# Optimization experiments

Hardware: AMD Instinct MI355X
Metric: run time of the kernel (lower is better)

## Reference

```python
import jax, jax.numpy as jnp
import numpy as np


def _l2norm(t, axis=-1, eps=1e-12):
    # matches torch F.normalize: x / max(||x||, eps)
    n = jnp.sqrt(jnp.sum(t * t, axis=axis, keepdims=True))
    return t / jnp.maximum(n, eps)


def setup_inputs() -> dict:
    key = jax.random.key(0)
    ks = jax.random.split(key, 5)
    B, N, C, H = 16, 4096, 768, 12
    x = jax.random.normal(ks[0], (B, N, C), dtype=jnp.float32)
    Wqkv = jax.random.normal(ks[1], (C, 3 * C), dtype=jnp.float32) * (C ** -0.5)
    bqkv = jax.random.normal(ks[2], (3 * C,), dtype=jnp.float32) * 0.02
    Wproj = jax.random.normal(ks[3], (C, C), dtype=jnp.float32) * (C ** -0.5)
    bproj = jax.random.normal(ks[4], (C,), dtype=jnp.float32) * 0.02
    temperature = jnp.ones((H, 1, 1), dtype=jnp.float32)
    return {"x": x, "Wqkv": Wqkv, "bqkv": bqkv, "Wproj": Wproj,
            "bproj": bproj, "temperature": temperature}


def reference(x, Wqkv, bqkv, Wproj, bproj, temperature):
    B, N, C = x.shape
    H = temperature.shape[0]
    Dh = C // H
    qkv = x @ Wqkv + bqkv                      # [B,N,3C]
    qkv = qkv.reshape(B, N, 3, H, Dh)
    # -> [3,B,H,Dh,N] (channels-as-tokens layout)
    qkv = jnp.transpose(qkv, (2, 0, 3, 4, 1))
    q, k, v = qkv[0], qkv[1], qkv[2]           # each [B,H,Dh,N]
    q = _l2norm(q, axis=-1)
    k = _l2norm(k, axis=-1)
    # cross-covariance over channels: [B,H,Dh,Dh]
    attn = jnp.einsum('bhdn,bhen->bhde', q, k) * temperature
    attn = jax.nn.softmax(attn, axis=-1)
    out = jnp.einsum('bhde,bhen->bhdn', attn, v)  # [B,H,Dh,N]
    out = jnp.transpose(out, (0, 3, 1, 2)).reshape(B, N, C)
    return out @ Wproj + bproj
```

## Files before the change

kernel.cpp:

```cpp
#include <hip/hip_runtime.h>

typedef __bf16 bf16x8 __attribute__((ext_vector_type(8)));
typedef float  f32x4  __attribute__((ext_vector_type(4)));
typedef unsigned short u16x8 __attribute__((ext_vector_type(8)));
typedef unsigned short u16x4 __attribute__((ext_vector_type(4)));

#define MFMA16(a, b, c) __builtin_amdgcn_mfma_f32_16x16x32_bf16((a), (b), (c), 0, 0, 0)

#define GLOAD16(g, l) __builtin_amdgcn_global_load_lds( \
    (const __attribute__((address_space(1))) void*)(g),  \
    (__attribute__((address_space(3))) void*)(l), 16, 0, 0)

__device__ __forceinline__ float bf2f(unsigned short u) {
    unsigned int x = ((unsigned int)u) << 16;
    return __builtin_bit_cast(float, x);
}
__device__ __forceinline__ unsigned short f2bf(float f) {
    unsigned int x = __builtin_bit_cast(unsigned int, f);
    x = x + 0x7FFFu + ((x >> 16) & 1u);
    return (unsigned short)(x >> 16);
}
__device__ __forceinline__ bool is_f32(const unsigned short* tf) { return tf[0] == 0; }
__device__ __forceinline__ float ldscal(const void* p, int i, bool f32m) {
    return f32m ? ((const float*)p)[i] : bf2f(((const unsigned short*)p)[i]);
}

__global__ __launch_bounds__(256)
void conv_x(const void* __restrict__ in, unsigned short* __restrict__ out,
            const unsigned short* __restrict__ tf)
{
    const bool f32m = is_f32(tf);
    const int n8 = 6291456;
    for (int i = blockIdx.x * 256 + threadIdx.x; i < n8; i += gridDim.x * 256) {
        u16x8 v;
        if (f32m) {
            const float* p = (const float*)in + (size_t)i * 8;
            f32x4 a = *(const f32x4*)p;
            f32x4 b = *(const f32x4*)(p + 4);
#pragma unroll
            for (int j = 0; j < 4; ++j) { v[j] = f2bf(a[j]); v[4 + j] = f2bf(b[j]); }
        } else {
            v = *(const u16x8*)((const unsigned short*)in + (size_t)i * 8);
        }
        *(u16x8*)&out[(size_t)i * 8] = v;
    }
}

__global__ __launch_bounds__(256)
void tr_conv(const void* __restrict__ in_, unsigned short* __restrict__ out,
             int R, int C, int istride, const unsigned short* __restrict__ tf)
{
    __shared__ unsigned short T[64 * 72];
    const bool f32m = is_f32(tf);
    const int nct = C >> 6;
    const int tx = blockIdx.x % nct;
    const int ty = blockIdx.x / nct;
    const int r0 = ty * 64, c0 = tx * 64;
    const int t = threadIdx.x;
#pragma unroll
    for (int s = 0; s < 2; ++s) {
        const int idx = t + s * 256;
        const int rr = idx >> 3;
        const int cc = (idx & 7) * 8;
        unsigned short v[8];
        if (f32m) {
            const float* inf = (const float*)in_;
            f32x4 a = *(const f32x4*)&inf[(size_t)(r0 + rr) * istride + c0 + cc];
            f32x4 b = *(const f32x4*)&inf[(size_t)(r0 + rr) * istride + c0 + cc + 4];
#pragma unroll
            for (int j = 0; j < 4; ++j) { v[j] = f2bf(a[j]); v[4 + j] = f2bf(b[j]); }
        } else {
            u16x8 a = *(const u16x8*)&((const unsigned short*)in_)[(size_t)(r0 + rr) * istride + c0 + cc];
#pragma unroll
            for (int j = 0; j < 8; ++j) v[j] = a[j];
        }
#pragma unroll
        for (int j = 0; j < 8; ++j) T[(cc + j) * 72 + rr] = v[j];
    }
    __syncthreads();
#pragma unroll
    for (int s = 0; s < 2; ++s) {
        const int idx = t + s * 256;
        const int cc = idx >> 3;
        const int rr = (idx & 7) * 8;
        u16x8 v = *(const u16x8*)&T[cc * 72 + rr];
        *(u16x8*)&out[(size_t)(c0 + cc) * R + r0 + rr] = v;
    }
}

__global__ __launch_bounds__(256)
void conv_wv(const void* __restrict__ Wqkv, unsigned short* __restrict__ Wv_bf,
             const unsigned short* __restrict__ tf)
{
    const bool f32m = is_f32(tf);
    const int t = blockIdx.x * 256 + threadIdx.x;
    const int c = t / 96;
    const int e0 = (t % 96) * 8;
    u16x8 v;
    if (f32m) {
        const float* p = (const float*)Wqkv + (size_t)c * 2304 + 1536 + e0;
        f32x4 a = *(const f32x4*)p;
        f32x4 b = *(const f32x4*)(p + 4);
#pragma unroll
        for (int j = 0; j < 4; ++j) { v[j] = f2bf(a[j]); v[4 + j] = f2bf(b[j]); }
    } else {
        v = *(const u16x8*)&((const unsigned short*)Wqkv)[(size_t)c * 2304 + 1536 + e0];
    }
    *(u16x8*)&Wv_bf[(size_t)c * 768 + e0] = v;
}

template<int MODE>
__global__ __launch_bounds__(512, 2)
void gemm256(const unsigned short* __restrict__ A,
             const unsigned short* __restrict__ BT,
             const void* __restrict__ bias,
             unsigned short* __restrict__ o0,
             unsigned short* __restrict__ o1,
             float* __restrict__ oF,
             const unsigned short* __restrict__ tf)
{
    constexpr int K = 768, NT = 12;
    constexpr int NB = (MODE == 0) ? 6 : 3;
    constexpr int LDSSZ = (MODE == 0) ? 135168 : 131072;
    __shared__ __align__(16) char SM[LDSSZ];

    const bool f32m = is_f32(tf);
    const int tid  = threadIdx.x;
    const int wave = tid >> 6;
    const int lane = tid & 63;
    const int wm   = wave >> 2;
    const int wn   = wave & 3;
    const int lr   = lane & 15;
    const int lq   = lane >> 4;
    const int sw16 = ((lq ^ (lr & 3)) << 4);

    const int per = gridDim.x >> 3;
    const int wg  = (blockIdx.x & 7) * per + (blockIdx.x >> 3);
    const int mt  = wg / NB;
    const int nt  = wg % NB;
    const size_t m0 = (size_t)mt * 256;
    const int n0 = nt * 256;

    const unsigned short* Bt = BT + ((MODE == 1) ? ((m0 >> 12) * (size_t)589824) : (size_t)0);

    f32x4 zero = {0.f, 0.f, 0.f, 0.f};
    f32x4 acc[8][4];
#pragma unroll
    for (int i = 0; i < 8; ++i)
#pragma unroll
        for (int j = 0; j < 4; ++j) acc[i][j] = zero;

    auto STAGE_EV = [&](int mat, int kh, int t) {
        const unsigned short* g = mat ? (Bt + (size_t)n0 * K) : (A + m0 * K);
        char* dst = SM + (t & 1) * 65536 + mat * 32768 + kh * 16384;
#pragma unroll
        for (int ev = 0; ev < 2; ++ev) {
            const int c = ev * 512 + tid;
            const int row = c >> 2;
            const int sg  = (c & 3) ^ (row & 3);
            GLOAD16(g + (size_t)row * K + t * 64 + kh * 32 + sg * 8, dst + c * 16);
        }
    };

    STAGE_EV(0, 0, 0); STAGE_EV(1, 0, 0);
    STAGE_EV(0, 1, 0); STAGE_EV(1, 1, 0);
    STAGE_EV(0, 0, 1); STAGE_EV(1, 0, 1);

    bf16x8 af[4], bfr[4];

#define READ_B(ks) do { \
    _Pragma("unroll") for (int ni = 0; ni < 4; ++ni) \
        bfr[ni] = *(const bf16x8*)(lb + (ks) * 16384 + (wn * 64 + ni * 16 + lr) * 64 + sw16); } while (0)
#define READ_A(mh, ks) do { \
    _Pragma("unroll") for (int mi = 0; mi < 4; ++mi) \
        af[mi] = *(const bf16x8*)(la + (ks) * 16384 + (wm * 128 + (mh) * 64 + mi * 16 + lr) * 64 + sw16); } while (0)
#define MFMA_Q(mh) do { \
    _Pragma("unroll") for (int mi = 0; mi < 4; ++mi) \
    _Pragma("unroll") for (int ni = 0; ni < 4; ++ni) \
        acc[(mh) * 4 + mi][ni] = MFMA16(af[mi], bfr[ni], acc[(mh) * 4 + mi][ni]); } while (0)
#define PH_MID() do { \
    __builtin_amdgcn_sched_barrier(0); \
    __builtin_amdgcn_s_barrier(); \
    asm volatile("s_waitcnt lgkmcnt(0)" ::: "memory"); \
    __builtin_amdgcn_sched_barrier(0); } while (0)
#define PH_END() do { \
    __builtin_amdgcn_sched_barrier(0); \
    __builtin_amdgcn_s_barrier(); } while (0)

    for (int t = 0; t < NT; ++t) {
        const char* la = (const char*)SM + (t & 1) * 65536;
        const char* lb = la + 32768;

        if (t < NT - 1) asm volatile("s_waitcnt vmcnt(8)" ::: "memory");
        else            asm volatile("s_waitcnt vmcnt(4)" ::: "memory");
        __builtin_amdgcn_s_barrier();
        __builtin_amdgcn_sched_barrier(0);

        READ_B(0); READ_A(0, 0);
        if (t + 1 < NT) STAGE_EV(0, 1, t + 1);
        PH_MID();
        __builtin_amdgcn_s_setprio(1); MFMA_Q(0); __builtin_amdgcn_s_setprio(0);
        PH_END();

        READ_A(1, 0);
        if (t + 1 < NT) STAGE_EV(1, 1, t + 1);
        if (t < NT - 1) asm volatile("s_waitcnt vmcnt(8)" ::: "memory");
        else            asm volatile("s_waitcnt vmcnt(0)" ::: "memory");
        PH_MID();
        __builtin_amdgcn_s_setprio(1); MFMA_Q(1); __builtin_amdgcn_s_setprio(0);
        PH_END();

        READ_B(1); READ_A(0, 1);
        if (t + 2 < NT) STAGE_EV(0, 0, t + 2);
        PH_MID();
        __builtin_amdgcn_s_setprio(1); MFMA_Q(0); __builtin_amdgcn_s_setprio(0);
        PH_END();

        READ_A(1, 1);
        if (t + 2 < NT) STAGE_EV(1, 0, t + 2);
        PH_MID();
        __builtin_amdgcn_s_setprio(1); MFMA_Q(1); __builtin_amdgcn_s_setprio(0);
        PH_END();
    }
#undef READ_B
#undef READ_A
#undef MFMA_Q
#undef PH_MID
#undef PH_END

    asm volatile("s_waitcnt lgkmcnt(0)" ::: "memory");
    __builtin_amdgcn_s_barrier();

    float bb[4];
#pragma unroll
    for (int ni = 0; ni < 4; ++ni) {
        const int col = n0 + wn * 64 + ni * 16 + lr;
        if (MODE == 0)      bb[ni] = ldscal(bias, col, f32m);
        else if (MODE == 1) bb[ni] = ((const float*)bias)[(m0 >> 12) * 768 + col];
        else                bb[ni] = 0.f;
    }

    if (MODE == 1 || MODE == 2) {
#pragma unroll
        for (int mi = 0; mi < 8; ++mi)
#pragma unroll
            for (int ni = 0; ni < 4; ++ni)
#pragma unroll
                for (int r = 0; r < 4; ++r) {
                    const size_t row = m0 + (size_t)(wm * 128 + mi * 16 + lq * 4 + r);
                    const int col = n0 + wn * 64 + ni * 16 + lr;
                    const float val = acc[mi][ni][r] + bb[ni];
                    if (MODE == 2)      o0[row * 768 + col] = f2bf(val);
                    else if (f32m)      oF[row * 768 + col] = val;
                    else                o0[row * 768 + col] = f2bf(val);
                }
    } else {
        unsigned short* CTw = (unsigned short*)SM + wave * (64 * 132);
        const int cbase = (n0 < 768) ? n0 : (n0 - 768);
        unsigned short* dst = (n0 < 768) ? o0 : o1;
        const int h = (cbase >> 6) + wn;
        const size_t bh = (m0 >> 12) * 12 + h;
        const int tokbase = (int)(m0 & 4095) + wm * 128;
#pragma unroll
        for (int mi = 0; mi < 8; ++mi)
#pragma unroll
            for (int ni = 0; ni < 4; ++ni) {
                u16x4 pk;
#pragma unroll
                for (int r = 0; r < 4; ++r) pk[r] = f2bf(acc[mi][ni][r] + bb[ni]);
                *(u16x4*)&CTw[(ni * 16 + lr) * 132 + mi * 16 + lq * 4] = pk;
            }
#pragma unroll
        for (int rep = 0; rep < 16; ++rep) {
            const int d = rep * 4 + lq;
            u16x8 v = *(const u16x8*)&CTw[d * 132 + lr * 8];
            *(u16x8*)&dst[(bh * 64 + d) * 4096 + tokbase + lr * 8] = v;
        }
    }
}

__global__ __launch_bounds__(256)
void attn_sm(const unsigned short* __restrict__ qt,
             const unsigned short* __restrict__ ktb,
             const unsigned short* __restrict__ tf,
             unsigned short* __restrict__ attnT)
{
    __shared__ float S[64][64];
    __shared__ float nq[64];
    __shared__ float nk[64];
    const bool f32m = is_f32(tf);
    const int bh = blockIdx.x;
    const int h = bh % 12;
    const unsigned short* Q  = qt  + (size_t)bh * (64 * 4096);
    const unsigned short* Kp = ktb + (size_t)bh * (64 * 4096);
    const int tid = threadIdx.x;
    const int wave = tid >> 6;
    const int lane = tid & 63;
    if (tid < 64) { nq[tid] = 0.f; nk[tid] = 0.f; }

    f32x4 zero = {0.f, 0.f, 0.f, 0.f};
    f32x4 acc[4][4];
#pragma unroll
    for (int i = 0; i < 4; ++i)
#pragma unroll
        for (int j = 0; j < 4; ++j) acc[i][j] = zero;
    f32x4 gq[4], gk[4];
#pragma unroll
    for (int i = 0; i < 4; ++i) { gq[i] = zero; gk[i] = zero; }

    const int lr = lane & 15;
    const int lq = lane >> 4;
    const int lk = lq * 8;

    for (int it = 0; it < 32; ++it) {
        const int nb = (it * 4 + wave) * 32 + lk;
        u16x8 qa[4], ka[4];
#pragma unroll
        for (int mi = 0; mi < 4; ++mi)
            qa[mi] = *(const u16x8*)&Q[(size_t)(mi * 16 + lr) * 4096 + nb];
#pragma unroll
        for (int ni = 0; ni < 4; ++ni)
            ka[ni] = *(const u16x8*)&Kp[(size_t)(ni * 16 + lr) * 4096 + nb];
#pragma unroll
        for (int mi = 0; mi < 4; ++mi) {
            gq[mi] = MFMA16(__builtin_bit_cast(bf16x8, qa[mi]),
                            __builtin_bit_cast(bf16x8, qa[mi]), gq[mi]);
            gk[mi] = MFMA16(__builtin_bit_cast(bf16x8, ka[mi]),
                            __builtin_bit_cast(bf16x8, ka[mi]), gk[mi]);
        }
#pragma unroll
        for (int mi = 0; mi < 4; ++mi)
#pragma unroll
            for (int ni = 0; ni < 4; ++ni)
                acc[mi][ni] = MFMA16(__builtin_bit_cast(bf16x8, qa[mi]),
                                     __builtin_bit_cast(bf16x8, ka[ni]),
                                     acc[mi][ni]);
    }

    for (int ww = 0; ww < 4; ++ww) {
        if (wave == ww) {
#pragma unroll
            for (int mi = 0; mi < 4; ++mi)
#pragma unroll
                for (int ni = 0; ni < 4; ++ni)
#pragma unroll
                    for (int r = 0; r < 4; ++r) {
                        const int d = mi * 16 + lq * 4 + r;
                        const int e = ni * 16 + lr;
                        if (ww == 0) S[d][e] = acc[mi][ni][r];
                        else         S[d][e] += acc[mi][ni][r];
                    }
        }
        __syncthreads();
    }

    {
        const int rdiag = lr - lq * 4;
        if (rdiag >= 0 && rdiag < 4) {
#pragma unroll
            for (int mi = 0; mi < 4; ++mi) {
                atomicAdd(&nq[mi * 16 + lr], gq[mi][rdiag]);
                atomicAdd(&nk[mi * 16 + lr], gk[mi][rdiag]);
            }
        }
    }
    __syncthreads();

    const int d  = tid >> 2;
    const int qq = tid & 3;
    const float tv = f32m ? ((const float*)tf)[h] : bf2f(tf[h]);
    const float qn = fmaxf(sqrtf(nq[d]), 1e-12f);
    float vals[16];
    float mx = -1e30f;
#pragma unroll
    for (int i = 0; i < 16; ++i) {
        const int e = qq * 16 + i;
        const float s = S[d][e] / (qn * fmaxf(sqrtf(nk[e]), 1e-12f)) * tv;
        vals[i] = s;
        mx = fmaxf(mx, s);
    }
    mx = fmaxf(mx, __shfl_xor(mx, 1));
    mx = fmaxf(mx, __shfl_xor(mx, 2));
    float sum = 0.f;
#pragma unroll
    for (int i = 0; i < 16; ++i) { vals[i] = __expf(vals[i] - mx); sum += vals[i]; }
    sum += __shfl_xor(sum, 1);
    sum += __shfl_xor(sum, 2);
    const float inv = 1.0f / sum;
#pragma unroll
    for (int i = 0; i < 16; ++i) {
        const int e = qq * 16 + i;
        attnT[(size_t)bh * 4096 + e * 64 + d] = f2bf(vals[i] * inv);
    }
}

__global__ __launch_bounds__(512)
void mb_build(const unsigned short* __restrict__ attnT,
              const unsigned short* __restrict__ WprojT,
              unsigned short* __restrict__ MbT)
{
    const int bh = blockIdx.x;
    const int b = bh / 12, h = bh % 12;
    const int tid = threadIdx.x;
    const int wave = tid >> 6;
    const int lane = tid & 63;
    const unsigned short* At = attnT + (size_t)bh * 4096;

    f32x4 zero = {0.f, 0.f, 0.f, 0.f};
    f32x4 acc[4][6];
#pragma unroll
    for (int i = 0; i < 4; ++i)
#pragma unroll
        for (int j = 0; j < 6; ++j) acc[i][j] = zero;

    const int lr  = lane & 15;
    const int lk8 = (lane >> 4) * 8;

#pragma unroll
    for (int ks = 0; ks < 2; ++ks) {
        bf16x8 af[4], bfr[6];
#pragma unroll
        for (int mi = 0; mi < 4; ++mi)
            af[mi] = *(const bf16x8*)&At[(mi * 16 + lr) * 64 + ks * 32 + lk8];
#pragma unroll
        for (int ni = 0; ni < 6; ++ni) {
            const int j = wave * 96 + ni * 16 + lr;
            bfr[ni] = *(const bf16x8*)&WprojT[(size_t)j * 768 + h * 64 + ks * 32 + lk8];
        }
#pragma unroll
        for (int mi = 0; mi < 4; ++mi)
#pragma unroll
            for (int ni = 0; ni < 6; ++ni)
                acc[mi][ni] = MFMA16(af[mi], bfr[ni], acc[mi][ni]);
    }

#pragma unroll
    for (int mi = 0; mi < 4; ++mi)
#pragma unroll
        for (int ni = 0; ni < 6; ++ni) {
            const int e = mi * 16 + (lane >> 4) * 4;
            const int j = wave * 96 + ni * 16 + lr;
            u16x4 pk;
#pragma unroll
            for (int r = 0; r < 4; ++r) pk[r] = f2bf(acc[mi][ni][r]);
            *(u16x4*)&MbT[(size_t)b * 589824 + (size_t)j * 768 + h * 64 + e] = pk;
        }
}

__global__ __launch_bounds__(256)
void beff_k(const unsigned short* __restrict__ MbT,
            const void* __restrict__ bqkv, const void* __restrict__ bp,
            float* __restrict__ beff, const unsigned short* __restrict__ tf)
{
    __shared__ float bv[768];
    const bool f32m = is_f32(tf);
    for (int i = threadIdx.x; i < 768; i += 256) bv[i] = ldscal(bqkv, 1536 + i, f32m);
    __syncthreads();
    const int t = blockIdx.x * 256 + threadIdx.x;
    const int b = t / 768, j = t % 768;
    float s = ldscal(bp, j, f32m);
    const unsigned short* row = MbT + (size_t)b * 589824 + (size_t)j * 768;
    for (int e8 = 0; e8 < 96; ++e8) {
        u16x8 m = *(const u16x8*)&row[e8 * 8];
#pragma unroll
        for (int jj = 0; jj < 8; ++jj) s += bf2f(m[jj]) * bv[e8 * 8 + jj];
    }
    beff[t] = s;
}

extern "C" void kernel_launch(void* const* d_in, const int* in_sizes, int n_in,
                              void* d_out, int out_size, void* d_ws, size_t ws_size,
                              hipStream_t stream)
{
    const void* x    = d_in[0];
    const void* Wqkv = d_in[1];
    const void* bqkv = d_in[2];
    const void* Wp   = d_in[3];
    const void* bp   = d_in[4];
    const unsigned short* tf = (const unsigned short*)d_in[5];

    char* w = (char*)d_ws;
    unsigned short* qt     = (unsigned short*)(w);
    unsigned short* PT     = (unsigned short*)(w);
    float*          beff   = (float*)(w + 18874368);
    unsigned short* ktb    = (unsigned short*)(w + 100663296);
    unsigned short* xb     = (unsigned short*)(w + 201326592);
    unsigned short* WqkT   = (unsigned short*)(w + 301989888);
    unsigned short* Wv_bf  = (unsigned short*)(w + 304349184);
    unsigned short* attnT  = (unsigned short*)(w + 305528832);
    unsigned short* MbT    = (unsigned short*)(w + 307101696);
    unsigned short* WprojT = (unsigned short*)(w + 325976064);

    conv_x <<<dim3(2048), dim3(256), 0, stream>>>(x, xb, tf);
    tr_conv<<<dim3(288),  dim3(256), 0, stream>>>(Wqkv, WqkT, 768, 1536, 2304, tf);
    conv_wv<<<dim3(288),  dim3(256), 0, stream>>>(Wqkv, Wv_bf, tf);
    tr_conv<<<dim3(144),  dim3(256), 0, stream>>>(Wp, WprojT, 768, 768, 768, tf);

    gemm256<0><<<dim3(1536), dim3(512), 0, stream>>>(xb, WqkT, bqkv, qt, ktb, nullptr, tf);
    attn_sm<<<dim3(192), dim3(256), 0, stream>>>(qt, ktb, tf, attnT);
    mb_build<<<dim3(192), dim3(512), 0, stream>>>(attnT, WprojT, MbT);
    gemm256<2><<<dim3(144), dim3(512), 0, stream>>>(MbT, Wv_bf, nullptr, PT, nullptr, nullptr, tf);
    beff_k<<<dim3(48), dim3(256), 0, stream>>>(MbT, bqkv, bp, beff, tf);
    gemm256<1><<<dim3(768), dim3(512), 0, stream>>>(xb, PT, beff,
        (unsigned short*)d_out, nullptr, (float*)d_out, tf);
}
```

Before: 473.2 us.

## Compute q·k cross-covariance via per-batch Gram matrix instead of materialising Q and K

```diff
diff --git a/kernel.cpp b/kernel.cpp
--- a/kernel.cpp
+++ b/kernel.cpp
@@ -26,23 +26,42 @@
 }
 
 __global__ __launch_bounds__(256)
-void conv_x(const void* __restrict__ in, unsigned short* __restrict__ out,
-            const unsigned short* __restrict__ tf)
-{
+void tr_dual(const void* __restrict__ in_, unsigned short* __restrict__ xb,
+             unsigned short* __restrict__ xbT, const unsigned short* __restrict__ tf)
+{
+    __shared__ unsigned short T[64 * 72];
     const bool f32m = is_f32(tf);
-    const int n8 = 6291456;
-    for (int i = blockIdx.x * 256 + threadIdx.x; i < n8; i += gridDim.x * 256) {
+    const int tx = blockIdx.x % 12;
+    const int ty = blockIdx.x / 12;
+    const int r0 = ty * 64, c0 = tx * 64;
+    const int t = threadIdx.x;
+#pragma unroll
+    for (int s = 0; s < 2; ++s) {
+        const int idx = t + s * 256;
+        const int rr = idx >> 3;
+        const int cc = (idx & 7) * 8;
         u16x8 v;
         if (f32m) {
-            const float* p = (const float*)in + (size_t)i * 8;
-            f32x4 a = *(const f32x4*)p;
-            f32x4 b = *(const f32x4*)(p + 4);
+            const float* inf = (const float*)in_;
+            f32x4 a = *(const f32x4*)&inf[(size_t)(r0 + rr) * 768 + c0 + cc];
+            f32x4 b = *(const f32x4*)&inf[(size_t)(r0 + rr) * 768 + c0 + cc + 4];
 #pragma unroll
             for (int j = 0; j < 4; ++j) { v[j] = f2bf(a[j]); v[4 + j] = f2bf(b[j]); }
         } else {
-            v = *(const u16x8*)((const unsigned short*)in + (size_t)i * 8);
-        }
-        *(u16x8*)&out[(size_t)i * 8] = v;
+            v = *(const u16x8*)&((const unsigned short*)in_)[(size_t)(r0 + rr) * 768 + c0 + cc];
+        }
+        *(u16x8*)&xb[(size_t)(r0 + rr) * 768 + c0 + cc] = v;
+#pragma unroll
+        for (int j = 0; j < 8; ++j) T[(cc + j) * 72 + rr] = v[j];
+    }
+    __syncthreads();
+#pragma unroll
+    for (int s = 0; s < 2; ++s) {
+        const int idx = t + s * 256;
+        const int cc = idx >> 3;
+        const int rr = (idx & 7) * 8;
+        u16x8 v = *(const u16x8*)&T[cc * 72 + rr];
+        *(u16x8*)&xbT[(size_t)(c0 + cc) * 65536 + r0 + rr] = v;
     }
 }
 
@@ -109,20 +128,40 @@
     *(u16x8*)&Wv_bf[(size_t)c * 768 + e0] = v;
 }
 
+__global__ __launch_bounds__(256)
+void colsum(const unsigned short* __restrict__ xbT, float* __restrict__ s)
+{
+    const int b = blockIdx.x / 12;
+    const int jg = blockIdx.x % 12;
+    const int tid = threadIdx.x;
+    const int d = tid >> 2;
+    const int seg = tid & 3;
+    const int j = jg * 64 + d;
+    const unsigned short* p = xbT + (size_t)j * 65536 + b * 4096 + seg * 1024;
+    float acc = 0.f;
+    for (int i = 0; i < 128; ++i) {
+        u16x8 v = *(const u16x8*)&p[i * 8];
+#pragma unroll
+        for (int k = 0; k < 8; ++k) acc += bf2f(v[k]);
+    }
+    acc += __shfl_xor(acc, 1);
+    acc += __shfl_xor(acc, 2);
+    if (seg == 0) s[b * 768 + j] = acc;
+}
+
 template<int MODE>
 __global__ __launch_bounds__(512, 2)
 void gemm256(const unsigned short* __restrict__ A,
              const unsigned short* __restrict__ BT,
-             const void* __restrict__ bias,
+             const float* __restrict__ bias,
              unsigned short* __restrict__ o0,
-             unsigned short* __restrict__ o1,
              float* __restrict__ oF,
              const unsigned short* __restrict__ tf)
 {
-    constexpr int K = 768, NT = 12;
-    constexpr int NB = (MODE == 0) ? 6 : 3;
-    constexpr int LDSSZ = (MODE == 0) ? 135168 : 131072;
-    __shared__ __align__(16) char SM[LDSSZ];
+    constexpr int NT = (MODE == 3) ? 64 : 12;
+    constexpr size_t LDA = (MODE == 3) ? 65536 : 768;
+    constexpr size_t LDB = (MODE == 3) ? 65536 : 768;
+    __shared__ __align__(16) char SM[131072];
 
     const bool f32m = is_f32(tf);
     const int tid  = threadIdx.x;
@@ -132,16 +171,28 @@
     const int wn   = wave & 3;
     const int lr   = lane & 15;
     const int lq   = lane >> 4;
-    const int sw16 = ((lq ^ (lr & 3)) << 4);
+    const int lrh  = lr >> 1;
+    const int pA   = (((lr & 1) << 2) | lq) ^ lrh;
 
     const int per = gridDim.x >> 3;
     const int wg  = (blockIdx.x & 7) * per + (blockIdx.x >> 3);
-    const int mt  = wg / NB;
-    const int nt  = wg % NB;
+    int b = 0, mt, nt;
+    if (MODE == 3)      { b = wg / 9;  const int r = wg % 9;  mt = r / 3; nt = r % 3; }
+    else if (MODE == 4) { b = wg / 18; const int r = wg % 18; mt = r / 3; nt = r % 3; }
+    else                { mt = wg / 3; nt = wg % 3; }
     const size_t m0 = (size_t)mt * 256;
     const int n0 = nt * 256;
 
-    const unsigned short* Bt = BT + ((MODE == 1) ? ((m0 >> 12) * (size_t)589824) : (size_t)0);
+    const unsigned short* Ab;
+    const unsigned short* Bb;
+    if (MODE == 3)      { Ab = A + m0 * LDA + (size_t)b * 4096;
+                          Bb = A + (size_t)n0 * LDA + (size_t)b * 4096; }
+    else if (MODE == 4) { Ab = A + m0 * LDA;
+                          Bb = BT + (size_t)b * 589824 + (size_t)n0 * LDB; }
+    else if (MODE == 1) { Ab = A + m0 * LDA;
+                          Bb = BT + (m0 >> 12) * (size_t)589824 + (size_t)n0 * LDB; }
+    else                { Ab = A + m0 * LDA;
+                          Bb = BT + (size_t)n0 * LDB; }
 
     f32x4 zero = {0.f, 0.f, 0.f, 0.f};
     f32x4 acc[8][4];
@@ -151,14 +202,17 @@
         for (int j = 0; j < 4; ++j) acc[i][j] = zero;
 
     auto STAGE_EV = [&](int mat, int kh, int t) {
-        const unsigned short* g = mat ? (Bt + (size_t)n0 * K) : (A + m0 * K);
+        const unsigned short* g = mat ? Bb : Ab;
+        const size_t ld = mat ? LDB : LDA;
         char* dst = SM + (t & 1) * 65536 + mat * 32768 + kh * 16384;
 #pragma unroll
         for (int ev = 0; ev < 2; ++ev) {
             const int c = ev * 512 + tid;
-            const int row = c >> 2;
-            const int sg  = (c & 3) ^ (row & 3);
-            GLOAD16(g + (size_t)row * K + t * 64 + kh * 32 + sg * 8, dst + c * 16);
+            const int rp = c >> 3;
+            const int chunk = (c & 7) ^ (rp & 7);
+            const int srow = rp * 2 + (chunk >> 2);
+            const int sk = kh * 32 + (chunk & 3) * 8;
+            GLOAD16(g + (size_t)srow * ld + t * 64 + sk, dst + c * 16);
         }
     };
 
@@ -170,10 +224,10 @@
 
 #define READ_B(ks) do { \
     _Pragma("unroll") for (int ni = 0; ni < 4; ++ni) \
-        bfr[ni] = *(const bf16x8*)(lb + (ks) * 16384 + (wn * 64 + ni * 16 + lr) * 64 + sw16); } while (0)
+        bfr[ni] = *(const bf16x8*)(lb + (ks) * 16384 + (wn * 32 + ni * 8 + lrh) * 128 + pA * 16); } while (0)
 #define READ_A(mh, ks) do { \
     _Pragma("unroll") for (int mi = 0; mi < 4; ++mi) \
-        af[mi] = *(const bf16x8*)(la + (ks) * 16384 + (wm * 128 + (mh) * 64 + mi * 16 + lr) * 64 + sw16); } while (0)
+        af[mi] = *(const bf16x8*)(la + (ks) * 16384 + (wm * 64 + (mh) * 32 + mi * 8 + lrh) * 128 + pA * 16); } while (0)
 #define MFMA_Q(mh) do { \
     _Pragma("unroll") for (int mi = 0; mi < 4; ++mi) \
     _Pragma("unroll") for (int ni = 0; ni < 4; ++ni) \
@@ -228,75 +282,62 @@
 #undef PH_MID
 #undef PH_END
 
-    asm volatile("s_waitcnt lgkmcnt(0)" ::: "memory");
-    __builtin_amdgcn_s_barrier();
-
     float bb[4];
 #pragma unroll
     for (int ni = 0; ni < 4; ++ni) {
         const int col = n0 + wn * 64 + ni * 16 + lr;
-        if (MODE == 0)      bb[ni] = ldscal(bias, col, f32m);
-        else if (MODE == 1) bb[ni] = ((const float*)bias)[(m0 >> 12) * 768 + col];
-        else                bb[ni] = 0.f;
-    }
-
-    if (MODE == 1 || MODE == 2) {
-#pragma unroll
-        for (int mi = 0; mi < 8; ++mi)
-#pragma unroll
-            for (int ni = 0; ni < 4; ++ni)
-#pragma unroll
-                for (int r = 0; r < 4; ++r) {
-                    const size_t row = m0 + (size_t)(wm * 128 + mi * 16 + lq * 4 + r);
-                    const int col = n0 + wn * 64 + ni * 16 + lr;
-                    const float val = acc[mi][ni][r] + bb[ni];
-                    if (MODE == 2)      o0[row * 768 + col] = f2bf(val);
-                    else if (f32m)      oF[row * 768 + col] = val;
-                    else                o0[row * 768 + col] = f2bf(val);
+        bb[ni] = (MODE == 1) ? bias[(m0 >> 12) * 768 + col] : 0.f;
+    }
+
+#pragma unroll
+    for (int mi = 0; mi < 8; ++mi)
+#pragma unroll
+        for (int ni = 0; ni < 4; ++ni)
+#pragma unroll
+            for (int r = 0; r < 4; ++r) {
+                const size_t row = m0 + (size_t)(wm * 128 + mi * 16 + lq * 4 + r);
+                const int col = n0 + wn * 64 + ni * 16 + lr;
+                const float val = acc[mi][ni][r] + bb[ni];
+                if (MODE == 1) {
+                    if (f32m) oF[row * 768 + col] = val;
+                    else      o0[row * 768 + col] = f2bf(val);
+                } else if (MODE == 2) {
+                    o0[row * 768 + col] = f2bf(val);
+                } else if (MODE == 3) {
+                    o0[(size_t)b * 589824 + row * 768 + col] = f2bf(val);
+                } else {
+                    o0[(size_t)b * 1179648 + row * 768 + col] = f2bf(val);
                 }
-    } else {
-        unsigned short* CTw = (unsigned short*)SM + wave * (64 * 132);
-        const int cbase = (n0 < 768) ? n0 : (n0 - 768);
-        unsigned short* dst = (n0 < 768) ? o0 : o1;
-        const int h = (cbase >> 6) + wn;
-        const size_t bh = (m0 >> 12) * 12 + h;
-        const int tokbase = (int)(m0 & 4095) + wm * 128;
-#pragma unroll
-        for (int mi = 0; mi < 8; ++mi)
-#pragma unroll
-            for (int ni = 0; ni < 4; ++ni) {
-                u16x4 pk;
-#pragma unroll
-                for (int r = 0; r < 4; ++r) pk[r] = f2bf(acc[mi][ni][r] + bb[ni]);
-                *(u16x4*)&CTw[(ni * 16 + lr) * 132 + mi * 16 + lq * 4] = pk;
             }
-#pragma unroll
-        for (int rep = 0; rep < 16; ++rep) {
-            const int d = rep * 4 + lq;
-            u16x8 v = *(const u16x8*)&CTw[d * 132 + lr * 8];
-            *(u16x8*)&dst[(bh * 64 + d) * 4096 + tokbase + lr * 8] = v;
-        }
-    }
 }
 
 __global__ __launch_bounds__(256)
-void attn_sm(const unsigned short* __restrict__ qt,
-             const unsigned short* __restrict__ ktb,
-             const unsigned short* __restrict__ tf,
-             unsigned short* __restrict__ attnT)
+void attn2(const unsigned short* __restrict__ P,
+           const unsigned short* __restrict__ WqkT,
+           const float* __restrict__ s,
+           const void* __restrict__ bqkv,
+           const unsigned short* __restrict__ tf,
+           unsigned short* __restrict__ attnT)
 {
     __shared__ float S[64][64];
-    __shared__ float nq[64];
-    __shared__ float nk[64];
+    __shared__ float nq[64], nk[64], uq[64], uk[64];
+    __shared__ float sb[768];
+    __shared__ float bkv[64];
     const bool f32m = is_f32(tf);
     const int bh = blockIdx.x;
-    const int h = bh % 12;
-    const unsigned short* Q  = qt  + (size_t)bh * (64 * 4096);
-    const unsigned short* Kp = ktb + (size_t)bh * (64 * 4096);
+    const int b = bh / 12, h = bh % 12;
+    const unsigned short* Pq = P + (size_t)b * 1179648 + (size_t)(h * 64) * 768;
+    const unsigned short* Pk = Pq + 768 * 768;
+    const unsigned short* Wq = WqkT + (size_t)(h * 64) * 768;
+    const unsigned short* Wk = Wq + 768 * 768;
     const int tid = threadIdx.x;
     const int wave = tid >> 6;
     const int lane = tid & 63;
-    if (tid < 64) { nq[tid] = 0.f; nk[tid] = 0.f; }
+    const int lr = lane & 15;
+    const int lq = lane >> 4;
+
+    for (int i = tid; i < 768; i += 256) sb[i] = s[b * 768 + i];
+    if (tid < 64) bkv[tid] = ldscal(bqkv, 768 + h * 64 + tid, f32m);
 
     f32x4 zero = {0.f, 0.f, 0.f, 0.f};
     f32x4 acc[4][4];
@@ -304,30 +345,16 @@
     for (int i = 0; i < 4; ++i)
 #pragma unroll
         for (int j = 0; j < 4; ++j) acc[i][j] = zero;
-    f32x4 gq[4], gk[4];
-#pragma unroll
-    for (int i = 0; i < 4; ++i) { gq[i] = zero; gk[i] = zero; }
-
-    const int lr = lane & 15;
-    const int lq = lane >> 4;
-    const int lk = lq * 8;
-
-    for (int it = 0; it < 32; ++it) {
-        const int nb = (it * 4 + wave) * 32 + lk;
+
+    for (int ks = 0; ks < 6; ++ks) {
+        const int j0 = wave * 192 + ks * 32 + lq * 8;
         u16x8 qa[4], ka[4];
 #pragma unroll
         for (int mi = 0; mi < 4; ++mi)
-            qa[mi] = *(const u16x8*)&Q[(size_t)(mi * 16 + lr) * 4096 + nb];
+            qa[mi] = *(const u16x8*)&Pq[(size_t)(mi * 16 + lr) * 768 + j0];
 #pragma unroll
         for (int ni = 0; ni < 4; ++ni)
-            ka[ni] = *(const u16x8*)&Kp[(size_t)(ni * 16 + lr) * 4096 + nb];
-#pragma unroll
-        for (int mi = 0; mi < 4; ++mi) {
-            gq[mi] = MFMA16(__builtin_bit_cast(bf16x8, qa[mi]),
-                            __builtin_bit_cast(bf16x8, qa[mi]), gq[mi]);
-            gk[mi] = MFMA16(__builtin_bit_cast(bf16x8, ka[mi]),
-                            __builtin_bit_cast(bf16x8, ka[mi]), gk[mi]);
-        }
+            ka[ni] = *(const u16x8*)&Wk[(size_t)(ni * 16 + lr) * 768 + j0];
 #pragma unroll
         for (int mi = 0; mi < 4; ++mi)
 #pragma unroll
@@ -336,6 +363,7 @@
                                      __builtin_bit_cast(bf16x8, ka[ni]),
                                      acc[mi][ni]);
     }
+    __syncthreads();
 
     for (int ww = 0; ww < 4; ++ww) {
         if (wave == ww) {
@@ -354,30 +382,55 @@
         __syncthreads();
     }
 
+    const int d  = tid >> 2;
+    const int q4 = tid & 3;
     {
-        const int rdiag = lr - lq * 4;
-        if (rdiag >= 0 && rdiag < 4) {
-#pragma unroll
-            for (int mi = 0; mi < 4; ++mi) {
-                atomicAdd(&nq[mi * 16 + lr], gq[mi][rdiag]);
-                atomicAdd(&nk[mi * 16 + lr], gk[mi][rdiag]);
+        const unsigned short* pqr = Pq + (size_t)d * 768 + q4 * 192;
+        const unsigned short* wqr = Wq + (size_t)d * 768 + q4 * 192;
+        const unsigned short* pkr = Pk + (size_t)d * 768 + q4 * 192;
+        const unsigned short* wkr = Wk + (size_t)d * 768 + q4 * 192;
+        float a_nq = 0.f, a_uq = 0.f, a_nk = 0.f, a_uk = 0.f;
+        for (int i = 0; i < 24; ++i) {
+            u16x8 vp = *(const u16x8*)&pqr[i * 8];
+            u16x8 vw = *(const u16x8*)&wqr[i * 8];
+            u16x8 kp = *(const u16x8*)&pkr[i * 8];
+            u16x8 kw = *(const u16x8*)&wkr[i * 8];
+#pragma unroll
+            for (int j = 0; j < 8; ++j) {
+                const float wqv = bf2f(vw[j]);
+                const float wkv = bf2f(kw[j]);
+                const float sj = sb[q4 * 192 + i * 8 + j];
+                a_nq += bf2f(vp[j]) * wqv;
+                a_uq += sj * wqv;
+                a_nk += bf2f(kp[j]) * wkv;
+                a_uk += sj * wkv;
             }
         }
+        a_nq += __shfl_xor(a_nq, 1); a_nq += __shfl_xor(a_nq, 2);
+        a_uq += __shfl_xor(a_uq, 1); a_uq += __shfl_xor(a_uq, 2);
+        a_nk += __shfl_xor(a_nk, 1); a_nk += __shfl_xor(a_nk, 2);
+        a_uk += __shfl_xor(a_uk, 1); a_uk += __shfl_xor(a_uk, 2);
+        if (q4 == 0) { nq[d] = a_nq; uq[d] = a_uq; nk[d] = a_nk; uk[d] = a_uk; }
     }
     __syncthreads();
 
-    const int d  = tid >> 2;
-    const int qq = tid & 3;
-    const float tv = f32m ? ((const float*)tf)[h] : bf2f(tf[h]);
-    const float qn = fmaxf(sqrtf(nq[d]), 1e-12f);
+    const float tv  = f32m ? ((const float*)tf)[h] : bf2f(tf[h]);
+    const float bqd = ldscal(bqkv, h * 64 + d, f32m);
+    const float uqd = uq[d];
+    const float nqf = nq[d] + 2.f * bqd * uqd + 4096.f * bqd * bqd;
+    const float qn  = fmaxf(sqrtf(fmaxf(nqf, 0.f)), 1e-12f);
     float vals[16];
     float mx = -1e30f;
 #pragma unroll
     for (int i = 0; i < 16; ++i) {
-        const int e = qq * 16 + i;
-        const float s = S[d][e] / (qn * fmaxf(sqrtf(nk[e]), 1e-12f)) * tv;
-        vals[i] = s;
-        mx = fmaxf(mx, s);
+        const int e = q4 * 16 + i;
+        const float bke = bkv[e];
+        const float nkf = nk[e] + 2.f * bke * uk[e] + 4096.f * bke * bke;
+        const float kn  = fmaxf(sqrtf(fmaxf(nkf, 0.f)), 1e-12f);
+        const float sv  = S[d][e] + bqd * uk[e] + uqd * bke + 4096.f * bqd * bke;
+        const float val = sv / (qn * kn) * tv;
+        vals[i] = val;
+        mx = fmaxf(mx, val);
     }
     mx = fmaxf(mx, __shfl_xor(mx, 1));
     mx = fmaxf(mx, __shfl_xor(mx, 2));
@@ -389,7 +442,7 @@
     const float inv = 1.0f / sum;
 #pragma unroll
     for (int i = 0; i < 16; ++i) {
-        const int e = qq * 16 + i;
+        const int e = q4 * 16 + i;
         attnT[(size_t)bh * 4096 + e * 64 + d] = f2bf(vals[i] * inv);
     }
 }
@@ -480,27 +533,31 @@
     const unsigned short* tf = (const unsigned short*)d_in[5];
 
     char* w = (char*)d_ws;
-    unsigned short* qt     = (unsigned short*)(w);
-    unsigned short* PT     = (unsigned short*)(w);
-    float*          beff   = (float*)(w + 18874368);
-    unsigned short* ktb    = (unsigned short*)(w + 100663296);
-    unsigned short* xb     = (unsigned short*)(w + 201326592);
-    unsigned short* WqkT   = (unsigned short*)(w + 301989888);
-    unsigned short* Wv_bf  = (unsigned short*)(w + 304349184);
-    unsigned short* attnT  = (unsigned short*)(w + 305528832);
-    unsigned short* MbT    = (unsigned short*)(w + 307101696);
-    unsigned short* WprojT = (unsigned short*)(w + 325976064);
-
-    conv_x <<<dim3(2048), dim3(256), 0, stream>>>(x, xb, tf);
+    unsigned short* xbT    = (unsigned short*)(w);
+    unsigned short* xb     = (unsigned short*)(w + 100663296);
+    unsigned short* G      = (unsigned short*)(w + 201326592);
+    unsigned short* P      = (unsigned short*)(w + 220200960);
+    unsigned short* PT     = (unsigned short*)(w + 257949696);
+    unsigned short* MbT    = (unsigned short*)(w + 276824064);
+    unsigned short* WqkT   = (unsigned short*)(w + 295698432);
+    unsigned short* Wv_bf  = (unsigned short*)(w + 298057728);
+    unsigned short* WprojT = (unsigned short*)(w + 299237376);
+    unsigned short* attnT  = (unsigned short*)(w + 300417024);
+    float*          sB     = (float*)(w + 301989888);
+    float*          beff   = (float*)(w + 302039040);
+
+    tr_dual<<<dim3(12288), dim3(256), 0, stream>>>(x, xb, xbT, tf);
     tr_conv<<<dim3(288),  dim3(256), 0, stream>>>(Wqkv, WqkT, 768, 1536, 2304, tf);
     conv_wv<<<dim3(288),  dim3(256), 0, stream>>>(Wqkv, Wv_bf, tf);
     tr_conv<<<dim3(144),  dim3(256), 0, stream>>>(Wp, WprojT, 768, 768, 768, tf);
-
-    gemm256<0><<<dim3(1536), dim3(512), 0, stream>>>(xb, WqkT, bqkv, qt, ktb, nullptr, tf);
-    attn_sm<<<dim3(192), dim3(256), 0, stream>>>(qt, ktb, tf, attnT);
+    colsum <<<dim3(192),  dim3(256), 0, stream>>>(xbT, sB);
+
+    gemm256<3><<<dim3(144), dim3(512), 0, stream>>>(xbT, nullptr, nullptr, G, nullptr, tf);
+    gemm256<4><<<dim3(288), dim3(512), 0, stream>>>(WqkT, G, nullptr, P, nullptr, tf);
+    attn2<<<dim3(192), dim3(256), 0, stream>>>(P, WqkT, sB, bqkv, tf, attnT);
     mb_build<<<dim3(192), dim3(512), 0, stream>>>(attnT, WprojT, MbT);
-    gemm256<2><<<dim3(144), dim3(512), 0, stream>>>(MbT, Wv_bf, nullptr, PT, nullptr, nullptr, tf);
+    gemm256<2><<<dim3(144), dim3(512), 0, stream>>>(MbT, Wv_bf, nullptr, PT, nullptr, tf);
     beff_k<<<dim3(48), dim3(256), 0, stream>>>(MbT, bqkv, bp, beff, tf);
     gemm256<1><<<dim3(768), dim3(512), 0, stream>>>(xb, PT, beff,
-        (unsigned short*)d_out, nullptr, (float*)d_out, tf);
-}
+        (unsigned short*)d_out, (float*)d_out, tf);
+}
```

After: 453.8 us. 4.1% less time.
